# Optimization experiments

Hardware: AMD Instinct MI355X
Metric: run time of the kernel (lower is better)

Reference implementation:

```python
import jax, jax.numpy as jnp
import numpy as np

C_M, C_Z, C = 256, 128, 32
N_SEQ, N_RES = 128, 256


def setup_inputs() -> dict:
    key = jax.random.key(0)
    ks = jax.random.split(key, 9)
    s = 0.02
    return {
        "m": jax.random.normal(ks[0], (N_SEQ, N_RES, C_M), dtype=jnp.float32),
        "ln_w": jnp.ones((C_M,), dtype=jnp.float32),
        "ln_b": jnp.zeros((C_M,), dtype=jnp.float32),
        "w1": jax.random.normal(ks[1], (C, C_M), dtype=jnp.float32) * s,
        "b1": jnp.zeros((C,), dtype=jnp.float32),
        "w2": jax.random.normal(ks[2], (C, C_M), dtype=jnp.float32) * s,
        "b2": jnp.zeros((C,), dtype=jnp.float32),
        "wo": jax.random.normal(ks[3], (C_Z, C * C), dtype=jnp.float32) * s,
        "bo": jnp.zeros((C_Z,), dtype=jnp.float32),
    }


def reference(m, ln_w, ln_b, w1, b1, w2, b2, wo, bo):
    n_seq = m.shape[-3]
    # LayerNorm over c_m
    mu = jnp.mean(m, axis=-1, keepdims=True)
    var = jnp.mean(jnp.square(m - mu), axis=-1, keepdims=True)
    mn = (m - mu) * jax.lax.rsqrt(var + 1e-5) * ln_w + ln_b
    # dual projections to c channels: [s, i, c]
    a = jnp.einsum('sim,cm->sic', mn, w1) + b1
    b = jnp.einsum('sjm,dm->sjd', mn, w2) + b2
    # outer product mean contracted over sequence axis: [i, j, c, d]
    o = jnp.einsum('sic,sjd->ijcd', a, b)
    o = o.reshape(o.shape[0], o.shape[1], C * C)
    # output projection and mean over sequences
    z = (jnp.einsum('ijk,zk->ijz', o, wo) + bo) / n_seq
    return z
```

## Files before the change

### kernel.cpp

```cpp
#include <hip/hip_runtime.h>
#include <hip/hip_bf16.h>
#include <stdint.h>

#define N_RES 256
#define CMDIM 256

typedef __attribute__((ext_vector_type(8))) short bf16x8;
typedef __attribute__((ext_vector_type(4))) float f32x4;
typedef __attribute__((ext_vector_type(2))) unsigned int u32x2;

__device__ __forceinline__ unsigned short f32_to_bf16(float f) {
    union { float f; unsigned int u; } v; v.f = f;
    unsigned int u = v.u;
    return (unsigned short)((u + 0x7FFFu + ((u >> 16) & 1u)) >> 16);
}

__device__ __forceinline__ int swz5(int x) {
    return ((x >> 2) & 7) | (((x >> 5) & 1) << 3) | ((x & 1) << 4);
}


__global__ __launch_bounds__(256) void k_prep(
    const float* __restrict__ w1, const float* __restrict__ w2,
    const float* __restrict__ wo,
    unsigned short* __restrict__ Wbf, unsigned short* __restrict__ wof)
{
    int t = blockIdx.x * 256 + threadIdx.x;
    if (t < 16384) {
        int ch = t >> 8, cm = t & 255;
        float v = (ch < 32) ? w1[ch * 256 + cm] : w2[(ch - 32) * 256 + cm];
        int addr = ((ch >> 4) * 8 + (cm >> 5)) * 512 + ((cm >> 3) & 3) * 128 + (ch & 15) * 8 + (cm & 7);
        Wbf[addr] = f32_to_bf16(v);
    }
    if (t < 131072) {
        int zo = t >> 10, k = t & 1023;
        int addr = ((zo >> 4) * 32 + (k >> 5)) * 512 + ((k >> 3) & 3) * 128 + (zo & 15) * 8 + (k & 7);
        wof[addr] = f32_to_bf16(wo[t]);
    }
}

__global__ __launch_bounds__(256) void k_ln_proj(
    const float* __restrict__ m, const float* __restrict__ lnw, const float* __restrict__ lnb,
    const float* __restrict__ b1, const float* __restrict__ b2,
    const unsigned short* __restrict__ Wbf,
    unsigned short* __restrict__ A2f, unsigned short* __restrict__ B2f)
{
    __shared__ unsigned short mn[32 * 256];
    __shared__ unsigned short stg[2048];
    int b = blockIdx.x;
    int i = b >> 2, sblk = b & 3;
    int tid = threadIdx.x;
    int wv = tid >> 6, lane = tid & 63;
    int quad = lane >> 4, l15 = lane & 15;

    f32x4 lw = *(const f32x4*)(lnw + lane * 4);
    f32x4 lb = *(const f32x4*)(lnb + lane * 4);

    #pragma unroll
    for (int r = 0; r < 8; ++r) {
        int sl = wv * 8 + r;
        int s = sblk * 32 + sl;
        const float* row = m + ((size_t)s * N_RES + i) * CMDIM;
        f32x4 x = *(const f32x4*)(row + lane * 4);
        float s1 = x[0] + x[1] + x[2] + x[3];
        float s2 = x[0]*x[0] + x[1]*x[1] + x[2]*x[2] + x[3]*x[3];
        #pragma unroll
        for (int off = 32; off; off >>= 1) {
            s1 += __shfl_xor(s1, off);
            s2 += __shfl_xor(s2, off);
        }
        float mu = s1 * (1.0f / 256.0f);
        float var = s2 * (1.0f / 256.0f) - mu * mu;
        float rstd = rsqrtf(var + 1e-5f);
        float n0 = (x[0] - mu) * rstd * lw[0] + lb[0];
        float n1 = (x[1] - mu) * rstd * lw[1] + lb[1];
        float n2 = (x[2] - mu) * rstd * lw[2] + lb[2];
        float n3 = (x[3] - mu) * rstd * lw[3] + lb[3];
        unsigned int p0 = (unsigned)f32_to_bf16(n0) | ((unsigned)f32_to_bf16(n1) << 16);
        unsigned int p1 = (unsigned)f32_to_bf16(n2) | ((unsigned)f32_to_bf16(n3) << 16);
        int chunk = lane >> 1;
        int pos = (chunk & 16) | ((chunk ^ sl) & 15);
        unsigned int* dst = (unsigned int*)((char*)mn + sl * 512 + pos * 16 + (lane & 1) * 8);
        dst[0] = p0; dst[1] = p1;
    }
    __syncthreads();

    bf16x8 af[8];
    #pragma unroll
    for (int ks = 0; ks < 8; ++ks)
        af[ks] = *(const bf16x8*)(Wbf + (wv * 8 + ks) * 512 + lane * 8);

    f32x4 acc[2];
    acc[0] = (f32x4){0.f, 0.f, 0.f, 0.f};
    acc[1] = (f32x4){0.f, 0.f, 0.f, 0.f};
    #pragma unroll
    for (int ks = 0; ks < 8; ++ks) {
        #pragma unroll
        for (int nb = 0; nb < 2; ++nb) {
            int sl = nb * 16 + l15;
            int chunk = ks * 4 + quad;
            int pos = (chunk & 16) | ((chunk ^ sl) & 15);
            bf16x8 bf = *(const bf16x8*)((char*)mn + sl * 512 + pos * 16);
            acc[nb] = __builtin_amdgcn_mfma_f32_16x16x32_bf16(af[ks], bf, acc[nb], 0, 0, 0);
        }
    }

    const float* bsrc = (wv < 2) ? b1 : b2;
    f32x4 bias = *(const f32x4*)(bsrc + (wv & 1) * 16 + quad * 4);
    unsigned short* sbase = stg + (wv >> 1) * 1024 + (wv & 1) * 512 + quad * 32;
    #pragma unroll
    for (int nb = 0; nb < 2; ++nb) {
        int sl = nb * 16 + l15;
        int soff = ((sl >> 3) & 3) * 128 + (sl & 7);
        #pragma unroll
        for (int reg = 0; reg < 4; ++reg)
            sbase[soff + reg * 8] = f32_to_bf16(acc[nb][reg] + bias[reg]);
    }
    __syncthreads();

    int part = tid >> 7, blk = (tid >> 6) & 1, l = tid & 63;
    unsigned short* gdst = (part ? B2f : A2f) + ((i * 2 + blk) * 4 + sblk) * 512 + l * 8;
    *(bf16x8*)gdst = *(const bf16x8*)(stg + tid * 8);
}

__global__ __launch_bounds__(256, 2) void k_fused(
    const unsigned short* __restrict__ A2f, const unsigned short* __restrict__ B2f,
    const unsigned short* __restrict__ wof, const float* __restrict__ bo,
    float* __restrict__ out)
{
    __shared__ char olds[65536];
    int bid = blockIdx.x;
    int sb = (bid & 7) * 256 + (bid >> 3);
    int bx = sb & 63, by = sb >> 6;
    int tid = threadIdx.x, wv = tid >> 6, lane = tid & 63;
    int quad = lane >> 4, l15 = lane & 15;
    int wm = wv & 1, wn = wv >> 1;

    const unsigned short* Abase = A2f + (size_t)((bx * 8 + wn * 4) * 4) * 512 + lane * 8;

    bf16x8 bn[4][4];
    #pragma unroll
    for (int nb = 0; nb < 4; ++nb)
        #pragma unroll
        for (int ks = 0; ks < 4; ++ks)
            bn[ks][nb] = *(const bf16x8*)(Abase + (size_t)(nb * 4 + ks) * 512);

    #pragma unroll
    for (int pass = 0; pass < 2; ++pass) {
        const unsigned short* Bbase = B2f + (size_t)((by * 16 + pass * 8 + wm * 4) * 4) * 512 + lane * 8;
        f32x4 acc[4][4];
        #pragma unroll
        for (int a = 0; a < 4; ++a)
            #pragma unroll
            for (int b = 0; b < 4; ++b) acc[a][b] = (f32x4){0.f, 0.f, 0.f, 0.f};

        bf16x8 am[4][4];
        #pragma unroll
        for (int mb = 0; mb < 4; ++mb)
            #pragma unroll
            for (int ks = 0; ks < 4; ++ks)
                am[ks][mb] = *(const bf16x8*)(Bbase + (size_t)(mb * 4 + ks) * 512);

        __builtin_amdgcn_s_setprio(1);
        #pragma unroll
        for (int ks = 0; ks < 4; ++ks)
            #pragma unroll
            for (int mb = 0; mb < 4; ++mb)
                #pragma unroll
                for (int nb = 0; nb < 4; ++nb)
                    acc[mb][nb] = __builtin_amdgcn_mfma_f32_16x16x32_bf16(am[ks][mb], bn[ks][nb], acc[mb][nb], 0, 0, 0);
        __builtin_amdgcn_s_setprio(0);

        #pragma unroll
        for (int mb = 0; mb < 4; ++mb) {
            int m_ = wm * 64 + mb * 16 + quad * 4;
            int d0 = m_ & 31;
            int jl = pass * 4 + (m_ >> 5);
            #pragma unroll
            for (int nb = 0; nb < 4; ++nb) {
                int n_ = wn * 64 + nb * 16 + l15;
                int c = n_ & 31, il = n_ >> 5;
                int pair = il * 8 + jl;
                int e0 = c * 32 + d0;
                int chunk = e0 >> 3;
                int phys = pair ^ swz5(chunk);
                f32x4 a4 = acc[mb][nb];
                unsigned int p0 = (unsigned)f32_to_bf16(a4[0]) | ((unsigned)f32_to_bf16(a4[1]) << 16);
                unsigned int p1 = (unsigned)f32_to_bf16(a4[2]) | ((unsigned)f32_to_bf16(a4[3]) << 16);
                u32x2 pv = {p0, p1};
                *(u32x2*)(olds + chunk * 512 + phys * 16 + (e0 & 7) * 2) = pv;
            }
        }
    }

    int zg = wv;
    const unsigned short* wbase = wof + (size_t)(zg * 64) * 512 + lane * 8;

    bf16x8 af2[4][4], bfr2[4][4];
    #pragma unroll
    for (int p = 0; p < 3; ++p)
        #pragma unroll
        for (int zb = 0; zb < 2; ++zb)
            #pragma unroll
            for (int h = 0; h < 2; ++h)
                af2[p][zb * 2 + h] = *(const bf16x8*)(wbase + (size_t)(zb * 32 + 2 * p + h) * 512);

    __syncthreads();

    #pragma unroll
    for (int p = 0; p < 3; ++p)
        #pragma unroll
        for (int pb = 0; pb < 2; ++pb)
            #pragma unroll
            for (int h = 0; h < 2; ++h) {
                int kt = 2 * p + h;
                int pair = pb * 16 + l15;
                int chunk = kt * 4 + quad;
                int phys = pair ^ swz5(chunk);
                bfr2[p][pb * 2 + h] = *(const bf16x8*)(olds + chunk * 512 + phys * 16);
            }

    f32x4 acc2[2][2];
    #pragma unroll
    for (int a = 0; a < 2; ++a)
        #pragma unroll
        for (int b = 0; b < 2; ++b) acc2[a][b] = (f32x4){0.f, 0.f, 0.f, 0.f};

    #pragma unroll
    for (int s = 0; s < 16; ++s) {
        int slot = s & 3;
        if (s < 13) {
            int t = s + 3, ps = t & 3;
            #pragma unroll
            for (int zb = 0; zb < 2; ++zb)
                #pragma unroll
                for (int h = 0; h < 2; ++h)
                    af2[ps][zb * 2 + h] = *(const bf16x8*)(wbase + (size_t)(zb * 32 + 2 * t + h) * 512);
            #pragma unroll
            for (int pb = 0; pb < 2; ++pb)
                #pragma unroll
                for (int h = 0; h < 2; ++h) {
                    int kt = 2 * t + h;
                    int pair = pb * 16 + l15;
                    int chunk = kt * 4 + quad;
                    int phys = pair ^ swz5(chunk);
                    bfr2[ps][pb * 2 + h] = *(const bf16x8*)(olds + chunk * 512 + phys * 16);
                }
        }
        __builtin_amdgcn_s_setprio(1);
        #pragma unroll
        for (int h = 0; h < 2; ++h)
            #pragma unroll
            for (int zb = 0; zb < 2; ++zb)
                #pragma unroll
                for (int pb = 0; pb < 2; ++pb)
                    acc2[zb][pb] = __builtin_amdgcn_mfma_f32_16x16x32_bf16(
                        af2[slot][zb * 2 + h], bfr2[slot][pb * 2 + h], acc2[zb][pb], 0, 0, 0);
        __builtin_amdgcn_s_setprio(0);
    }

    #pragma unroll
    for (int zb = 0; zb < 2; ++zb) {
        int zo = zg * 32 + zb * 16 + quad * 4;
        f32x4 b4 = *(const f32x4*)(bo + zo);
        #pragma unroll
        for (int pb = 0; pb < 2; ++pb) {
            int pair = pb * 16 + l15;
            int i = bx * 4 + (pair >> 3);
            int j = by * 8 + (pair & 7);
            f32x4 v;
            #pragma unroll
            for (int reg = 0; reg < 4; ++reg)
                v[reg] = (acc2[zb][pb][reg] + b4[reg]) * (1.0f / 128.0f);
            *(f32x4*)(out + ((size_t)(i * 256 + j)) * 128 + zo) = v;
        }
    }
}

extern "C" void kernel_launch(void* const* d_in, const int* in_sizes, int n_in,
                              void* d_out, int out_size, void* d_ws, size_t ws_size,
                              hipStream_t stream) {
    const float* m   = (const float*)d_in[0];
    const float* lnw = (const float*)d_in[1];
    const float* lnb = (const float*)d_in[2];
    const float* w1  = (const float*)d_in[3];
    const float* b1  = (const float*)d_in[4];
    const float* w2  = (const float*)d_in[5];
    const float* b2  = (const float*)d_in[6];
    const float* wo  = (const float*)d_in[7];
    const float* bo  = (const float*)d_in[8];
    float* out = (float*)d_out;
    char* ws = (char*)d_ws;

    unsigned short* Wbf = (unsigned short*)(ws);
    unsigned short* wof = (unsigned short*)(ws + 32768);
    unsigned short* A2f = (unsigned short*)(ws + 32768 + 262144);
    unsigned short* B2f = (unsigned short*)(ws + 32768 + 262144 + 2097152);

    hipLaunchKernelGGL(k_prep, dim3(512), dim3(256), 0, stream, w1, w2, wo, Wbf, wof);
    hipLaunchKernelGGL(k_ln_proj, dim3(1024), dim3(256), 0, stream,
                       m, lnw, lnb, b1, b2, Wbf, A2f, B2f);
    hipLaunchKernelGGL(k_fused, dim3(2048), dim3(256), 0, stream,
                       A2f, B2f, wof, bo, out);
}
```

Before: 141.6 us.

## Double fused kernel block to 512 threads, split passes and K across waves

The fused outer-product/projection kernel now uses 8 waves per block instead of 4. The two outer-product passes run concurrently on separate wave groups instead of sequentially. The output projection's K dimension is split in half across wave pairs, and the partial sums are reduced through shared memory. This is meant to raise parallelism and latency hiding per block and shorten each wave's serial work, at the cost of an extra LDS reduction with two more barriers and possibly lower occupancy, since launch bounds now request 512 threads with 2 blocks.

```diff
diff --git a/kernel.cpp b/kernel.cpp
--- a/kernel.cpp
+++ b/kernel.cpp
@@ -123,7 +123,7 @@
     *(bf16x8*)gdst = *(const bf16x8*)(stg + tid * 8);
 }
 
-__global__ __launch_bounds__(256, 2) void k_fused(
+__global__ __launch_bounds__(512, 2) void k_fused(
     const unsigned short* __restrict__ A2f, const unsigned short* __restrict__ B2f,
     const unsigned short* __restrict__ wof, const float* __restrict__ bo,
     float* __restrict__ out)
@@ -134,86 +134,81 @@
     int bx = sb & 63, by = sb >> 6;
     int tid = threadIdx.x, wv = tid >> 6, lane = tid & 63;
     int quad = lane >> 4, l15 = lane & 15;
-    int wm = wv & 1, wn = wv >> 1;
+    int pass = wv >> 2, wm = (wv >> 1) & 1, wn = wv & 1;
 
     const unsigned short* Abase = A2f + (size_t)((bx * 8 + wn * 4) * 4) * 512 + lane * 8;
-
-    bf16x8 bn[4][4];
+    const unsigned short* Bbase = B2f + (size_t)((by * 16 + pass * 8 + wm * 4) * 4) * 512 + lane * 8;
+
+    bf16x8 bn[4][4], am[4][4];
     #pragma unroll
     for (int nb = 0; nb < 4; ++nb)
         #pragma unroll
         for (int ks = 0; ks < 4; ++ks)
             bn[ks][nb] = *(const bf16x8*)(Abase + (size_t)(nb * 4 + ks) * 512);
-
-    #pragma unroll
-    for (int pass = 0; pass < 2; ++pass) {
-        const unsigned short* Bbase = B2f + (size_t)((by * 16 + pass * 8 + wm * 4) * 4) * 512 + lane * 8;
-        f32x4 acc[4][4];
-        #pragma unroll
-        for (int a = 0; a < 4; ++a)
-            #pragma unroll
-            for (int b = 0; b < 4; ++b) acc[a][b] = (f32x4){0.f, 0.f, 0.f, 0.f};
-
-        bf16x8 am[4][4];
+    #pragma unroll
+    for (int mb = 0; mb < 4; ++mb)
+        #pragma unroll
+        for (int ks = 0; ks < 4; ++ks)
+            am[ks][mb] = *(const bf16x8*)(Bbase + (size_t)(mb * 4 + ks) * 512);
+
+    f32x4 acc[4][4];
+    #pragma unroll
+    for (int a = 0; a < 4; ++a)
+        #pragma unroll
+        for (int b = 0; b < 4; ++b) acc[a][b] = (f32x4){0.f, 0.f, 0.f, 0.f};
+
+    __builtin_amdgcn_s_setprio(1);
+    #pragma unroll
+    for (int ks = 0; ks < 4; ++ks)
         #pragma unroll
         for (int mb = 0; mb < 4; ++mb)
             #pragma unroll
-            for (int ks = 0; ks < 4; ++ks)
-                am[ks][mb] = *(const bf16x8*)(Bbase + (size_t)(mb * 4 + ks) * 512);
-
-        __builtin_amdgcn_s_setprio(1);
-        #pragma unroll
-        for (int ks = 0; ks < 4; ++ks)
-            #pragma unroll
-            for (int mb = 0; mb < 4; ++mb)
-                #pragma unroll
-                for (int nb = 0; nb < 4; ++nb)
-                    acc[mb][nb] = __builtin_amdgcn_mfma_f32_16x16x32_bf16(am[ks][mb], bn[ks][nb], acc[mb][nb], 0, 0, 0);
-        __builtin_amdgcn_s_setprio(0);
-
-        #pragma unroll
-        for (int mb = 0; mb < 4; ++mb) {
-            int m_ = wm * 64 + mb * 16 + quad * 4;
-            int d0 = m_ & 31;
-            int jl = pass * 4 + (m_ >> 5);
-            #pragma unroll
-            for (int nb = 0; nb < 4; ++nb) {
-                int n_ = wn * 64 + nb * 16 + l15;
-                int c = n_ & 31, il = n_ >> 5;
-                int pair = il * 8 + jl;
-                int e0 = c * 32 + d0;
-                int chunk = e0 >> 3;
-                int phys = pair ^ swz5(chunk);
-                f32x4 a4 = acc[mb][nb];
-                unsigned int p0 = (unsigned)f32_to_bf16(a4[0]) | ((unsigned)f32_to_bf16(a4[1]) << 16);
-                unsigned int p1 = (unsigned)f32_to_bf16(a4[2]) | ((unsigned)f32_to_bf16(a4[3]) << 16);
-                u32x2 pv = {p0, p1};
-                *(u32x2*)(olds + chunk * 512 + phys * 16 + (e0 & 7) * 2) = pv;
-            }
-        }
-    }
-
-    int zg = wv;
+            for (int nb = 0; nb < 4; ++nb)
+                acc[mb][nb] = __builtin_amdgcn_mfma_f32_16x16x32_bf16(am[ks][mb], bn[ks][nb], acc[mb][nb], 0, 0, 0);
+    __builtin_amdgcn_s_setprio(0);
+
+    #pragma unroll
+    for (int mb = 0; mb < 4; ++mb) {
+        int m_ = wm * 64 + mb * 16 + quad * 4;
+        int d0 = m_ & 31;
+        int jl = pass * 4 + (m_ >> 5);
+        #pragma unroll
+        for (int nb = 0; nb < 4; ++nb) {
+            int n_ = wn * 64 + nb * 16 + l15;
+            int c = n_ & 31, il = n_ >> 5;
+            int pair = il * 8 + jl;
+            int e0 = c * 32 + d0;
+            int chunk = e0 >> 3;
+            int phys = pair ^ swz5(chunk);
+            f32x4 a4 = acc[mb][nb];
+            unsigned int p0 = (unsigned)f32_to_bf16(a4[0]) | ((unsigned)f32_to_bf16(a4[1]) << 16);
+            unsigned int p1 = (unsigned)f32_to_bf16(a4[2]) | ((unsigned)f32_to_bf16(a4[3]) << 16);
+            u32x2 pv = {p0, p1};
+            *(u32x2*)(olds + chunk * 512 + phys * 16 + (e0 & 7) * 2) = pv;
+        }
+    }
+
+    int zg = wv >> 1, kh = wv & 1, kt0 = kh * 16;
     const unsigned short* wbase = wof + (size_t)(zg * 64) * 512 + lane * 8;
 
-    bf16x8 af2[4][4], bfr2[4][4];
-    #pragma unroll
-    for (int p = 0; p < 3; ++p)
+    bf16x8 af2[3][4], bfr2[3][4];
+    #pragma unroll
+    for (int p = 0; p < 2; ++p)
         #pragma unroll
         for (int zb = 0; zb < 2; ++zb)
             #pragma unroll
             for (int h = 0; h < 2; ++h)
-                af2[p][zb * 2 + h] = *(const bf16x8*)(wbase + (size_t)(zb * 32 + 2 * p + h) * 512);
-
-    __syncthreads();
-
-    #pragma unroll
-    for (int p = 0; p < 3; ++p)
+                af2[p][zb * 2 + h] = *(const bf16x8*)(wbase + (size_t)(zb * 32 + kt0 + 2 * p + h) * 512);
+
+    __syncthreads();
+
+    #pragma unroll
+    for (int p = 0; p < 2; ++p)
         #pragma unroll
         for (int pb = 0; pb < 2; ++pb)
             #pragma unroll
             for (int h = 0; h < 2; ++h) {
-                int kt = 2 * p + h;
+                int kt = kt0 + 2 * p + h;
                 int pair = pb * 16 + l15;
                 int chunk = kt * 4 + quad;
                 int phys = pair ^ swz5(chunk);
@@ -227,20 +222,20 @@
         for (int b = 0; b < 2; ++b) acc2[a][b] = (f32x4){0.f, 0.f, 0.f, 0.f};
 
     #pragma unroll
-    for (int s = 0; s < 16; ++s) {
-        int slot = s & 3;
-        if (s < 13) {
-            int t = s + 3, ps = t & 3;
+    for (int s = 0; s < 8; ++s) {
+        int slot = s % 3;
+        if (s < 6) {
+            int t = s + 2, ps = t % 3;
             #pragma unroll
             for (int zb = 0; zb < 2; ++zb)
                 #pragma unroll
                 for (int h = 0; h < 2; ++h)
-                    af2[ps][zb * 2 + h] = *(const bf16x8*)(wbase + (size_t)(zb * 32 + 2 * t + h) * 512);
+                    af2[ps][zb * 2 + h] = *(const bf16x8*)(wbase + (size_t)(zb * 32 + kt0 + 2 * t + h) * 512);
             #pragma unroll
             for (int pb = 0; pb < 2; ++pb)
                 #pragma unroll
                 for (int h = 0; h < 2; ++h) {
-                    int kt = 2 * t + h;
+                    int kt = kt0 + 2 * t + h;
                     int pair = pb * 16 + l15;
                     int chunk = kt * 4 + quad;
                     int phys = pair ^ swz5(chunk);
@@ -259,20 +254,33 @@
         __builtin_amdgcn_s_setprio(0);
     }
 
-    #pragma unroll
-    for (int zb = 0; zb < 2; ++zb) {
-        int zo = zg * 32 + zb * 16 + quad * 4;
-        f32x4 b4 = *(const f32x4*)(bo + zo);
-        #pragma unroll
-        for (int pb = 0; pb < 2; ++pb) {
-            int pair = pb * 16 + l15;
-            int i = bx * 4 + (pair >> 3);
-            int j = by * 8 + (pair & 7);
-            f32x4 v;
-            #pragma unroll
-            for (int reg = 0; reg < 4; ++reg)
-                v[reg] = (acc2[zb][pb][reg] + b4[reg]) * (1.0f / 128.0f);
-            *(f32x4*)(out + ((size_t)(i * 256 + j)) * 128 + zo) = v;
+    __syncthreads();
+    f32x4* red = (f32x4*)olds;
+    if (kh == 1) {
+        #pragma unroll
+        for (int zb = 0; zb < 2; ++zb)
+            #pragma unroll
+            for (int pb = 0; pb < 2; ++pb)
+                red[(((zg * 2 + zb) * 2 + pb) << 6) + quad * 16 + l15] = acc2[zb][pb];
+    }
+    __syncthreads();
+    if (kh == 0) {
+        #pragma unroll
+        for (int zb = 0; zb < 2; ++zb) {
+            int zo = zg * 32 + zb * 16 + quad * 4;
+            f32x4 b4 = *(const f32x4*)(bo + zo);
+            #pragma unroll
+            for (int pb = 0; pb < 2; ++pb) {
+                f32x4 part = red[(((zg * 2 + zb) * 2 + pb) << 6) + quad * 16 + l15];
+                int pair = pb * 16 + l15;
+                int i = bx * 4 + (pair >> 3);
+                int j = by * 8 + (pair & 7);
+                f32x4 v;
+                #pragma unroll
+                for (int reg = 0; reg < 4; ++reg)
+                    v[reg] = (acc2[zb][pb][reg] + part[reg] + b4[reg]) * (1.0f / 128.0f);
+                *(f32x4*)(out + ((size_t)(i * 256 + j)) * 128 + zo) = v;
+            }
         }
     }
 }
@@ -300,6 +308,6 @@
     hipLaunchKernelGGL(k_prep, dim3(512), dim3(256), 0, stream, w1, w2, wo, Wbf, wof);
     hipLaunchKernelGGL(k_ln_proj, dim3(1024), dim3(256), 0, stream,
                        m, lnw, lnb, b1, b2, Wbf, A2f, B2f);
-    hipLaunchKernelGGL(k_fused, dim3(2048), dim3(256), 0, stream,
+    hipLaunchKernelGGL(k_fused, dim3(2048), dim3(512), 0, stream,
                        A2f, B2f, wof, bo, out);
 }
```

After: 149.3 us. 1.05x slower.

## Fold weight prep into LN-projection kernel and deepen output-GEMM prefetch

Applied to the files above, without the earlier changes.

Removes the separate k_prep launch. The wo bf16 conversion is spread across the LN/projection blocks, and w1/w2 are converted to bf16 MFMA fragments directly from fp32 in each wave. Separately, the output-projection loop's software pipeline grows from a 4-slot (3-ahead) to a 6-slot (5-ahead) prefetch with sched_barriers to pin instruction ordering. This saves one kernel launch and a dependency gap, at the cost of redundant w1/w2 conversion per block and higher register pressure in k_fused.

```diff
diff --git a/kernel.cpp b/kernel.cpp
--- a/kernel.cpp
+++ b/kernel.cpp
@@ -20,30 +20,13 @@
 }
 
 
-__global__ __launch_bounds__(256) void k_prep(
-    const float* __restrict__ w1, const float* __restrict__ w2,
-    const float* __restrict__ wo,
-    unsigned short* __restrict__ Wbf, unsigned short* __restrict__ wof)
-{
-    int t = blockIdx.x * 256 + threadIdx.x;
-    if (t < 16384) {
-        int ch = t >> 8, cm = t & 255;
-        float v = (ch < 32) ? w1[ch * 256 + cm] : w2[(ch - 32) * 256 + cm];
-        int addr = ((ch >> 4) * 8 + (cm >> 5)) * 512 + ((cm >> 3) & 3) * 128 + (ch & 15) * 8 + (cm & 7);
-        Wbf[addr] = f32_to_bf16(v);
-    }
-    if (t < 131072) {
-        int zo = t >> 10, k = t & 1023;
-        int addr = ((zo >> 4) * 32 + (k >> 5)) * 512 + ((k >> 3) & 3) * 128 + (zo & 15) * 8 + (k & 7);
-        wof[addr] = f32_to_bf16(wo[t]);
-    }
-}
-
 __global__ __launch_bounds__(256) void k_ln_proj(
     const float* __restrict__ m, const float* __restrict__ lnw, const float* __restrict__ lnb,
-    const float* __restrict__ b1, const float* __restrict__ b2,
-    const unsigned short* __restrict__ Wbf,
-    unsigned short* __restrict__ A2f, unsigned short* __restrict__ B2f)
+    const float* __restrict__ w1, const float* __restrict__ b1,
+    const float* __restrict__ w2, const float* __restrict__ b2,
+    const float* __restrict__ wo,
+    unsigned short* __restrict__ A2f, unsigned short* __restrict__ B2f,
+    unsigned short* __restrict__ wof)
 {
     __shared__ unsigned short mn[32 * 256];
     __shared__ unsigned short stg[2048];
@@ -52,6 +35,13 @@
     int tid = threadIdx.x;
     int wv = tid >> 6, lane = tid & 63;
     int quad = lane >> 4, l15 = lane & 15;
+
+    if (tid < 128) {
+        int t = b * 128 + tid;
+        int zo = t >> 10, k = t & 1023;
+        int addr = ((zo >> 4) * 32 + (k >> 5)) * 512 + ((k >> 3) & 3) * 128 + (zo & 15) * 8 + (k & 7);
+        wof[addr] = f32_to_bf16(wo[t]);
+    }
 
     f32x4 lw = *(const f32x4*)(lnw + lane * 4);
     f32x4 lb = *(const f32x4*)(lnb + lane * 4);
@@ -83,12 +73,27 @@
         unsigned int* dst = (unsigned int*)((char*)mn + sl * 512 + pos * 16 + (lane & 1) * 8);
         dst[0] = p0; dst[1] = p1;
     }
+
+    const float* wrow = (wv < 2) ? (w1 + (size_t)(wv * 16 + l15) * 256)
+                                 : (w2 + (size_t)((wv - 2) * 16 + l15) * 256);
+    bf16x8 af[8];
+    #pragma unroll
+    for (int ks = 0; ks < 8; ++ks) {
+        f32x4 lo = *(const f32x4*)(wrow + ks * 32 + quad * 8);
+        f32x4 hi = *(const f32x4*)(wrow + ks * 32 + quad * 8 + 4);
+        bf16x8 f;
+        f[0] = (short)f32_to_bf16(lo[0]);
+        f[1] = (short)f32_to_bf16(lo[1]);
+        f[2] = (short)f32_to_bf16(lo[2]);
+        f[3] = (short)f32_to_bf16(lo[3]);
+        f[4] = (short)f32_to_bf16(hi[0]);
+        f[5] = (short)f32_to_bf16(hi[1]);
+        f[6] = (short)f32_to_bf16(hi[2]);
+        f[7] = (short)f32_to_bf16(hi[3]);
+        af[ks] = f;
+    }
+
     __syncthreads();
-
-    bf16x8 af[8];
-    #pragma unroll
-    for (int ks = 0; ks < 8; ++ks)
-        af[ks] = *(const bf16x8*)(Wbf + (wv * 8 + ks) * 512 + lane * 8);
 
     f32x4 acc[2];
     acc[0] = (f32x4){0.f, 0.f, 0.f, 0.f};
@@ -196,19 +201,20 @@
     int zg = wv;
     const unsigned short* wbase = wof + (size_t)(zg * 64) * 512 + lane * 8;
 
-    bf16x8 af2[4][4], bfr2[4][4];
-    #pragma unroll
-    for (int p = 0; p < 3; ++p)
+    bf16x8 af2[6][4], bfr2[6][4];
+    #pragma unroll
+    for (int p = 0; p < 5; ++p)
         #pragma unroll
         for (int zb = 0; zb < 2; ++zb)
             #pragma unroll
             for (int h = 0; h < 2; ++h)
                 af2[p][zb * 2 + h] = *(const bf16x8*)(wbase + (size_t)(zb * 32 + 2 * p + h) * 512);
+    __builtin_amdgcn_sched_barrier(0);
 
     __syncthreads();
 
     #pragma unroll
-    for (int p = 0; p < 3; ++p)
+    for (int p = 0; p < 5; ++p)
         #pragma unroll
         for (int pb = 0; pb < 2; ++pb)
             #pragma unroll
@@ -219,6 +225,7 @@
                 int phys = pair ^ swz5(chunk);
                 bfr2[p][pb * 2 + h] = *(const bf16x8*)(olds + chunk * 512 + phys * 16);
             }
+    __builtin_amdgcn_sched_barrier(0);
 
     f32x4 acc2[2][2];
     #pragma unroll
@@ -228,9 +235,9 @@
 
     #pragma unroll
     for (int s = 0; s < 16; ++s) {
-        int slot = s & 3;
-        if (s < 13) {
-            int t = s + 3, ps = t & 3;
+        int slot = s % 6;
+        if (s < 11) {
+            int t = s + 5, ps = t % 6;
             #pragma unroll
             for (int zb = 0; zb < 2; ++zb)
                 #pragma unroll
@@ -246,6 +253,7 @@
                     int phys = pair ^ swz5(chunk);
                     bfr2[ps][pb * 2 + h] = *(const bf16x8*)(olds + chunk * 512 + phys * 16);
                 }
+            __builtin_amdgcn_sched_barrier(0);
         }
         __builtin_amdgcn_s_setprio(1);
         #pragma unroll
@@ -292,14 +300,12 @@
     float* out = (float*)d_out;
     char* ws = (char*)d_ws;
 
-    unsigned short* Wbf = (unsigned short*)(ws);
     unsigned short* wof = (unsigned short*)(ws + 32768);
     unsigned short* A2f = (unsigned short*)(ws + 32768 + 262144);
     unsigned short* B2f = (unsigned short*)(ws + 32768 + 262144 + 2097152);
 
-    hipLaunchKernelGGL(k_prep, dim3(512), dim3(256), 0, stream, w1, w2, wo, Wbf, wof);
     hipLaunchKernelGGL(k_ln_proj, dim3(1024), dim3(256), 0, stream,
-                       m, lnw, lnb, b1, b2, Wbf, A2f, B2f);
+                       m, lnw, lnb, w1, b1, w2, b2, wo, A2f, B2f, wof);
     hipLaunchKernelGGL(k_fused, dim3(2048), dim3(256), 0, stream,
                        A2f, B2f, wof, bo, out);
 }
```

After: 143.4 us. No clear change (+1.3%).
